# Performance work log

Hardware: AMD Instinct MI355X
Metric: run time of the kernel (lower is better)

Reference implementation:

```python
import jax, jax.numpy as jnp
import numpy as np

B, S, D_MODEL, D_K = 4, 4096, 1024, 64


def setup_inputs() -> dict:
    key = jax.random.key(0)
    kx, kq, kk, kv = jax.random.split(key, 4)
    x = jax.random.normal(kx, (B, S, D_MODEL), dtype=jnp.float32)
    # Linear(in, out) stores weight as (out, in); y = x @ W^T, no bias
    Wq = jax.random.normal(kq, (D_K, D_MODEL), dtype=jnp.float32) * (D_MODEL ** -0.5)
    Wk = jax.random.normal(kk, (D_K, D_MODEL), dtype=jnp.float32) * (D_MODEL ** -0.5)
    Wv = jax.random.normal(kv, (D_MODEL, D_MODEL), dtype=jnp.float32) * (D_MODEL ** -0.5)
    return {"x": x, "Wq": Wq, "Wk": Wk, "Wv": Wv}


def reference(x, Wq, Wk, Wv):
    # single-head scaled dot-product attention
    q = jnp.einsum('bsd,kd->bsk', x, Wq)   # [B,S,d_k]
    k = jnp.einsum('bsd,kd->bsk', x, Wk)   # [B,S,d_k]
    v = jnp.einsum('bsd,md->bsm', x, Wv)   # [B,S,d_model]
    scale = 1.0 / jnp.sqrt(jnp.asarray(q.shape[-1], q.dtype))
    scores = jnp.einsum('bqk,bsk->bqs', q, k) * scale  # [B,S,S]
    probs = jax.nn.softmax(scores, axis=-1)
    return jnp.einsum('bqs,bsm->bqm', probs, v)        # [B,S,d_model]
```

## Files before the change

kernel.cpp:

```cpp
#include <hip/hip_runtime.h>


#define DEV static __device__ __forceinline__

typedef __attribute__((ext_vector_type(8))) short bf16x8;
typedef __attribute__((ext_vector_type(4))) float f32x4;
typedef __attribute__((ext_vector_type(4))) unsigned short u16x4;
typedef __attribute__((ext_vector_type(8))) unsigned short u16x8;
typedef __attribute__((address_space(1))) void as1_void;
typedef __attribute__((address_space(3))) void as3_void;

DEV unsigned short f2bf(float f) {
  union { float f; unsigned u; } v; v.f = f;
  return (unsigned short)((v.u + 0x7FFFu + ((v.u >> 16) & 1u)) >> 16);
}

DEV unsigned pk_bf16(float a, float b) {
  union { float f; unsigned u; } va, vb;
  va.f = a; vb.f = b;
  return __builtin_amdgcn_perm(vb.u + 0x8000u, va.u + 0x8000u, 0x07060302u);
}

DEV void gload16(const void* g, void* l) {
  __builtin_amdgcn_global_load_lds((as1_void*)g, (as3_void*)l, 16, 0, 0);
}

DEV int swz(int row, int cb) { return (row << 7) + (cb ^ ((row & 7) << 4)); }

DEV void lgkm_barrier() {
  asm volatile("s_waitcnt lgkmcnt(0)" ::: "memory");
  __builtin_amdgcn_sched_barrier(0);
  __builtin_amdgcn_s_barrier();
  __builtin_amdgcn_sched_barrier(0);
}

__global__ __launch_bounds__(256) void cast_bf16_k(const float* __restrict__ in,
                                                   unsigned short* __restrict__ out,
                                                   int n8, float scale) {
  const int stride = gridDim.x * blockDim.x;
  for (int i = blockIdx.x * blockDim.x + threadIdx.x; i < n8; i += stride) {
    const float4* p = (const float4*)in + (size_t)i * 2;
    float4 a = p[0], b = p[1];
    u16x8 r;
    r[0] = f2bf(a.x * scale); r[1] = f2bf(a.y * scale);
    r[2] = f2bf(a.z * scale); r[3] = f2bf(a.w * scale);
    r[4] = f2bf(b.x * scale); r[5] = f2bf(b.y * scale);
    r[6] = f2bf(b.z * scale); r[7] = f2bf(b.w * scale);
    *(u16x8*)(out + (size_t)i * 8) = r;
  }
}

__global__ __launch_bounds__(256, 2) void gemm_qkv_k(
    const unsigned short* __restrict__ xb, const unsigned short* __restrict__ wcat,
    unsigned short* __restrict__ qk, unsigned short* __restrict__ vT) {
  __shared__ __align__(16) unsigned char smem[65536];
  unsigned char* sA = smem;
  unsigned char* sB = smem + 32768;
  const int tid = threadIdx.x;
  const int w = tid >> 6, lane = tid & 63, lo = lane & 15, hi = lane >> 4;
  const int wr = w >> 1, wc = w & 1;
  const int bn = blockIdx.x, m0 = blockIdx.y * 128, n0 = bn * 128;
  const char* aBase = (const char*)xb + (size_t)m0 * 2048;
  const char* bBase = (const char*)wcat + (size_t)n0 * 2048;

  const int soff = ((w * 4) << 10) + (lane << 4);
  f32x4 acc[4][4];
  const f32x4 z = {0.f, 0.f, 0.f, 0.f};
#pragma unroll
  for (int mi = 0; mi < 4; ++mi)
#pragma unroll
    for (int ni = 0; ni < 4; ++ni) acc[mi][ni] = z;

#pragma unroll
  for (int r2 = 0; r2 < 4; ++r2) {
    const int off = soff + (r2 << 10);
    const int row = off >> 7;
    const int cbs = (off & 127) ^ ((row & 7) << 4);
    gload16(aBase + (size_t)row * 2048 + cbs, sA + ((w * 4 + r2) << 10));
    gload16(bBase + (size_t)row * 2048 + cbs, sB + ((w * 4 + r2) << 10));
  }
  __syncthreads();

  int cur = 0;
  for (int k0 = 0; k0 < 1024; k0 += 64) {
    if (k0 + 64 < 1024) {
      const int nb = (cur ^ 1) * 16384;
#pragma unroll
      for (int r2 = 0; r2 < 4; ++r2) {
        const int off = soff + (r2 << 10);
        const int row = off >> 7;
        const int cbs = (off & 127) ^ ((row & 7) << 4);
        gload16(aBase + (size_t)row * 2048 + (k0 + 64) * 2 + cbs, sA + nb + ((w * 4 + r2) << 10));
        gload16(bBase + (size_t)row * 2048 + (k0 + 64) * 2 + cbs, sB + nb + ((w * 4 + r2) << 10));
      }
    }
    const int cb0 = cur * 16384;
#pragma unroll
    for (int kk = 0; kk < 2; ++kk) {
      const int cb = kk * 64 + hi * 16;
      bf16x8 af[4], bfv[4];
#pragma unroll
      for (int mi = 0; mi < 4; ++mi)
        af[mi] = *(const bf16x8*)(sA + cb0 + swz(wr * 64 + mi * 16 + lo, cb));
#pragma unroll
      for (int ni = 0; ni < 4; ++ni)
        bfv[ni] = *(const bf16x8*)(sB + cb0 + swz(wc * 64 + ni * 16 + lo, cb));
#pragma unroll
      for (int mi = 0; mi < 4; ++mi)
#pragma unroll
        for (int ni = 0; ni < 4; ++ni)
          acc[mi][ni] = __builtin_amdgcn_mfma_f32_16x16x32_bf16(af[mi], bfv[ni], acc[mi][ni], 0, 0, 0);
    }
    __syncthreads();
    cur ^= 1;
  }

  if (bn == 0) {
#pragma unroll
    for (int mi = 0; mi < 4; ++mi) {
      const int row = m0 + wr * 64 + mi * 16 + hi * 4;
#pragma unroll
      for (int ni = 0; ni < 4; ++ni) {
        const int col = wc * 64 + ni * 16 + lo;
#pragma unroll
        for (int r = 0; r < 4; ++r)
          qk[(size_t)(row + r) * 128 + col] = f2bf(acc[mi][ni][r]);
      }
    }
  } else {
#pragma unroll
    for (int mi = 0; mi < 4; ++mi) {
      const int grow = m0 + wr * 64 + mi * 16 + hi * 4;
      const int b = grow >> 12, s = grow & 4095;
#pragma unroll
      for (int ni = 0; ni < 4; ++ni) {
        const int vcol = (n0 - 128) + wc * 64 + ni * 16 + lo;
        u16x4 pk;
#pragma unroll
        for (int r = 0; r < 4; ++r) pk[r] = f2bf(acc[mi][ni][r]);
        *(u16x4*)(vT + (size_t)(b * 1024 + vcol) * 4096 + s) = pk;
      }
    }
  }
}

__global__ __launch_bounds__(512, 4) void pv_k(
    const unsigned short* __restrict__ qk, const unsigned short* __restrict__ vT,
    float* __restrict__ out) {
  __shared__ __align__(16) unsigned char smem[57344];
  unsigned char* sK = smem;
  unsigned char* sV = smem + 8192;
  unsigned char* sP = smem + 40960;
  const int tid = threadIdx.x;
  const int w = tid >> 6, lane = tid & 63, lo = lane & 15, hi = lane >> 4;
  const int wr = w >> 2, wc = w & 3;
  const int ck = blockIdx.x, qt = blockIdx.y, b = blockIdx.z;
  const char* qkB = (const char*)qk;
  const char* vTB = (const char*)vT;
  const size_t qrow0 = (size_t)(b * 4096 + qt * 128);
  const f32x4 z = {0.f, 0.f, 0.f, 0.f};

  const int q = w * 16 + lo;
  bf16x8 qf[2];
#pragma unroll
  for (int kk = 0; kk < 2; ++kk)
    qf[kk] = *(const bf16x8*)(qkB + (qrow0 + q) * 256 + kk * 64 + hi * 16);
  float lsum = 0.f;

  const int kc = w * 64 + lane;
  const int kRow = kc >> 3;
  const int kCbs = ((kc & 7) << 4) ^ ((kRow & 7) << 4);
  const char* kSrc = qkB + (size_t)(b * 4096 + kRow) * 256 + 128 + kCbs;

  const int g = lane & 3, dr = (lane >> 2) & 1, qq = lane >> 3;
  const int rr = (qq & 3) + ((qq >> 2) << 3) + (dr << 2);
  const int vRow0 = w * 16 + rr, vRow1 = vRow0 + 128;
  const char* vSrc0 = vTB + (size_t)(b * 1024 + ck * 256 + vRow0) * 8192 + g * 16;
  const char* vSrc1 = vTB + (size_t)(b * 1024 + ck * 256 + vRow1) * 8192 + g * 16;
  unsigned char* vDst0 = sV + vRow0 * 128;
  unsigned char* vDst1 = sV + vRow1 * 128;
  const int vX = g << 4, vR = (vRow0 & 7) << 4;

  const int qx7 = (q & 7) << 4;
  const int aP0 = (q << 7) + ((((hi >> 1) + 0) << 4) ^ qx7) + ((hi & 1) << 3);
  const int aP1 = (q << 7) + ((((hi >> 1) + 2) << 4) ^ qx7) + ((hi & 1) << 3);

  f32x4 acc[4][4];
#pragma unroll
  for (int mi = 0; mi < 4; ++mi)
#pragma unroll
    for (int ni = 0; ni < 4; ++ni) acc[mi][ni] = z;

  {
    float4 v0 = *(const float4*)(vSrc0);
    float4 v1 = *(const float4*)(vSrc1);
    if (w < 4) gload16(kSrc, sK + (w << 10));
    *(float4*)(vDst0 + (vX ^ vR)) = v0;
    *(float4*)(vDst1 + (vX ^ vR)) = v1;
  }
  __syncthreads();

  int cur = 0;
  for (int t = 0; t < 128; ++t) {
    float4 nv0, nv1;
    if (t < 127) {
      nv0 = *(const float4*)(vSrc0 + (size_t)(t + 1) * 64);
      nv1 = *(const float4*)(vSrc1 + (size_t)(t + 1) * 64);
      if (w < 4) gload16(kSrc + (size_t)(t + 1) * 8192, sK + (cur ^ 1) * 4096 + (w << 10));
    }
    f32x4 sv0 = z, sv1 = z;
#pragma unroll
    for (int kk = 0; kk < 2; ++kk) {
      bf16x8 kf0 = *(const bf16x8*)(sK + cur * 4096 + swz(lo, kk * 64 + hi * 16));
      bf16x8 kf1 = *(const bf16x8*)(sK + cur * 4096 + swz(16 + lo, kk * 64 + hi * 16));
      sv0 = __builtin_amdgcn_mfma_f32_16x16x32_bf16(kf0, qf[kk], sv0, 0, 0, 0);
      sv1 = __builtin_amdgcn_mfma_f32_16x16x32_bf16(kf1, qf[kk], sv1, 0, 0, 0);
    }
    {
      const float p0 = __builtin_amdgcn_exp2f(sv0[0]);
      const float p1 = __builtin_amdgcn_exp2f(sv0[1]);
      const float p2 = __builtin_amdgcn_exp2f(sv0[2]);
      const float p3 = __builtin_amdgcn_exp2f(sv0[3]);
      const float p4 = __builtin_amdgcn_exp2f(sv1[0]);
      const float p5 = __builtin_amdgcn_exp2f(sv1[1]);
      const float p6 = __builtin_amdgcn_exp2f(sv1[2]);
      const float p7 = __builtin_amdgcn_exp2f(sv1[3]);
      lsum += ((p0 + p1) + (p2 + p3)) + ((p4 + p5) + (p6 + p7));
      uint2 d0, d1;
      d0.x = pk_bf16(p0, p1); d0.y = pk_bf16(p2, p3);
      d1.x = pk_bf16(p4, p5); d1.y = pk_bf16(p6, p7);
      *(uint2*)(sP + aP0) = d0;
      *(uint2*)(sP + aP1) = d1;
    }
    lgkm_barrier();
    if (t < 127) {
      *(float4*)(vDst0 + ((((cur ^ 1) << 6) + vX) ^ vR)) = nv0;
      *(float4*)(vDst1 + ((((cur ^ 1) << 6) + vX) ^ vR)) = nv1;
    }
    __builtin_amdgcn_s_setprio(1);
    bf16x8 pa[4];
#pragma unroll
    for (int mi = 0; mi < 4; ++mi)
      pa[mi] = *(const bf16x8*)(sP + swz(wr * 64 + mi * 16 + lo, hi * 16));
#pragma unroll
    for (int ni = 0; ni < 4; ++ni) {
      bf16x8 vf = *(const bf16x8*)(sV + swz(wc * 64 + ni * 16 + lo, (cur << 6) + hi * 16));
#pragma unroll
      for (int mi = 0; mi < 4; ++mi)
        acc[mi][ni] = __builtin_amdgcn_mfma_f32_16x16x32_bf16(pa[mi], vf, acc[mi][ni], 0, 0, 0);
    }
    __builtin_amdgcn_s_setprio(0);
    __syncthreads();
    cur ^= 1;
  }

  lsum += __shfl_xor(lsum, 16, 64);
  lsum += __shfl_xor(lsum, 32, 64);
  float* lLds = (float*)smem;
  if (hi == 0) lLds[q] = lsum;
  __syncthreads();

#pragma unroll
  for (int mi = 0; mi < 4; ++mi)
#pragma unroll
    for (int r = 0; r < 4; ++r) {
      const int rloc = wr * 64 + mi * 16 + hi * 4 + r;
      const int grow = (int)qrow0 + rloc;
      const float linv = 1.0f / lLds[rloc];
#pragma unroll
      for (int ni = 0; ni < 4; ++ni) {
        const int col = ck * 256 + wc * 64 + ni * 16 + lo;
        out[(size_t)grow * 1024 + col] = acc[mi][ni][r] * linv;
      }
    }
}

extern "C" void kernel_launch(void* const* d_in, const int* in_sizes, int n_in,
                              void* d_out, int out_size, void* d_ws, size_t ws_size,
                              hipStream_t stream) {
  const float* x  = (const float*)d_in[0];
  const float* Wq = (const float*)d_in[1];
  const float* Wk = (const float*)d_in[2];
  const float* Wv = (const float*)d_in[3];

  char* ws = (char*)d_ws;
  unsigned short* xb    = (unsigned short*)(ws);
  unsigned short* wcat  = (unsigned short*)(ws + 33554432);
  unsigned short* qk    = (unsigned short*)(ws + 35913728);
  unsigned short* vT    = (unsigned short*)(ws + 40108032);

  const float SCALE_Q = 0.125f * 1.4426950408889634f;

  cast_bf16_k<<<2048, 256, 0, stream>>>(x, xb, 2097152, 1.0f);
  cast_bf16_k<<<32, 256, 0, stream>>>(Wq, wcat, 8192, SCALE_Q);
  cast_bf16_k<<<32, 256, 0, stream>>>(Wk, wcat + 65536, 8192, 1.0f);
  cast_bf16_k<<<512, 256, 0, stream>>>(Wv, wcat + 131072, 131072, 1.0f);

  gemm_qkv_k<<<dim3(9, 128), 256, 0, stream>>>(xb, wcat, qk, vT);
  pv_k<<<dim3(4, 32, 4), 512, 0, stream>>>(qk, vT, (float*)d_out);
}
```

Measured before the change: 253.3 us.

## Load V fragments directly into registers and remap blocks for XCD L2 locality

In the PV kernel, V tiles are no longer staged through shared memory. Each lane loads its MFMA B-operand fragments straight from global memory into double-buffered registers, which shrinks LDS from 56KB to 24KB and removes the LDS writes and reads for V. The grid is also flattened, and block indices are remapped so that blocks on the same XCD share the same (batch, column-chunk) group, meant to improve L2 reuse of K and V. The trade-off is that global loads are now less coalesced, since each lane reads 16 bytes from a different 8KB-strided row, and more registers are used.

```diff
diff --git a/kernel.cpp b/kernel.cpp
--- a/kernel.cpp
+++ b/kernel.cpp
@@ -147,14 +147,19 @@
 __global__ __launch_bounds__(512, 4) void pv_k(
     const unsigned short* __restrict__ qk, const unsigned short* __restrict__ vT,
     float* __restrict__ out) {
-  __shared__ __align__(16) unsigned char smem[57344];
+  __shared__ __align__(16) unsigned char smem[24576];
   unsigned char* sK = smem;
-  unsigned char* sV = smem + 8192;
-  unsigned char* sP = smem + 40960;
+  unsigned char* sP = smem + 8192;
   const int tid = threadIdx.x;
   const int w = tid >> 6, lane = tid & 63, lo = lane & 15, hi = lane >> 4;
   const int wr = w >> 2, wc = w & 3;
-  const int ck = blockIdx.x, qt = blockIdx.y, b = blockIdx.z;
+
+  const int flat = blockIdx.x;
+  const int xcd = flat & 7, slot = flat >> 3;
+  const int group = xcd + ((slot >> 5) << 3);
+  const int qt = slot & 31;
+  const int ck = group & 3, b = group >> 2;
+
   const char* qkB = (const char*)qk;
   const char* vTB = (const char*)vT;
   const size_t qrow0 = (size_t)(b * 4096 + qt * 128);
@@ -172,14 +177,10 @@
   const int kCbs = ((kc & 7) << 4) ^ ((kRow & 7) << 4);
   const char* kSrc = qkB + (size_t)(b * 4096 + kRow) * 256 + 128 + kCbs;
 
-  const int g = lane & 3, dr = (lane >> 2) & 1, qq = lane >> 3;
-  const int rr = (qq & 3) + ((qq >> 2) << 3) + (dr << 2);
-  const int vRow0 = w * 16 + rr, vRow1 = vRow0 + 128;
-  const char* vSrc0 = vTB + (size_t)(b * 1024 + ck * 256 + vRow0) * 8192 + g * 16;
-  const char* vSrc1 = vTB + (size_t)(b * 1024 + ck * 256 + vRow1) * 8192 + g * 16;
-  unsigned char* vDst0 = sV + vRow0 * 128;
-  unsigned char* vDst1 = sV + vRow1 * 128;
-  const int vX = g << 4, vR = (vRow0 & 7) << 4;
+  const char* vBase[4];
+#pragma unroll
+  for (int ni = 0; ni < 4; ++ni)
+    vBase[ni] = vTB + (size_t)(b * 1024 + ck * 256 + wc * 64 + ni * 16 + lo) * 8192 + hi * 16;
 
   const int qx7 = (q & 7) << 4;
   const int aP0 = (q << 7) + ((((hi >> 1) + 0) << 4) ^ qx7) + ((hi & 1) << 3);
@@ -191,68 +192,66 @@
 #pragma unroll
     for (int ni = 0; ni < 4; ++ni) acc[mi][ni] = z;
 
-  {
-    float4 v0 = *(const float4*)(vSrc0);
-    float4 v1 = *(const float4*)(vSrc1);
-    if (w < 4) gload16(kSrc, sK + (w << 10));
-    *(float4*)(vDst0 + (vX ^ vR)) = v0;
-    *(float4*)(vDst1 + (vX ^ vR)) = v1;
-  }
+  bf16x8 vA[4], vB[4];
+#pragma unroll
+  for (int ni = 0; ni < 4; ++ni) vA[ni] = *(const bf16x8*)(vBase[ni]);
+  if (w < 4) gload16(kSrc, sK + (w << 10));
   __syncthreads();
 
-  int cur = 0;
-  for (int t = 0; t < 128; ++t) {
-    float4 nv0, nv1;
-    if (t < 127) {
-      nv0 = *(const float4*)(vSrc0 + (size_t)(t + 1) * 64);
-      nv1 = *(const float4*)(vSrc1 + (size_t)(t + 1) * 64);
-      if (w < 4) gload16(kSrc + (size_t)(t + 1) * 8192, sK + (cur ^ 1) * 4096 + (w << 10));
-    }
-    f32x4 sv0 = z, sv1 = z;
-#pragma unroll
-    for (int kk = 0; kk < 2; ++kk) {
-      bf16x8 kf0 = *(const bf16x8*)(sK + cur * 4096 + swz(lo, kk * 64 + hi * 16));
-      bf16x8 kf1 = *(const bf16x8*)(sK + cur * 4096 + swz(16 + lo, kk * 64 + hi * 16));
-      sv0 = __builtin_amdgcn_mfma_f32_16x16x32_bf16(kf0, qf[kk], sv0, 0, 0, 0);
-      sv1 = __builtin_amdgcn_mfma_f32_16x16x32_bf16(kf1, qf[kk], sv1, 0, 0, 0);
-    }
-    {
-      const float p0 = __builtin_amdgcn_exp2f(sv0[0]);
-      const float p1 = __builtin_amdgcn_exp2f(sv0[1]);
-      const float p2 = __builtin_amdgcn_exp2f(sv0[2]);
-      const float p3 = __builtin_amdgcn_exp2f(sv0[3]);
-      const float p4 = __builtin_amdgcn_exp2f(sv1[0]);
-      const float p5 = __builtin_amdgcn_exp2f(sv1[1]);
-      const float p6 = __builtin_amdgcn_exp2f(sv1[2]);
-      const float p7 = __builtin_amdgcn_exp2f(sv1[3]);
-      lsum += ((p0 + p1) + (p2 + p3)) + ((p4 + p5) + (p6 + p7));
-      uint2 d0, d1;
-      d0.x = pk_bf16(p0, p1); d0.y = pk_bf16(p2, p3);
-      d1.x = pk_bf16(p4, p5); d1.y = pk_bf16(p6, p7);
-      *(uint2*)(sP + aP0) = d0;
-      *(uint2*)(sP + aP1) = d1;
-    }
-    lgkm_barrier();
-    if (t < 127) {
-      *(float4*)(vDst0 + ((((cur ^ 1) << 6) + vX) ^ vR)) = nv0;
-      *(float4*)(vDst1 + ((((cur ^ 1) << 6) + vX) ^ vR)) = nv1;
-    }
-    __builtin_amdgcn_s_setprio(1);
-    bf16x8 pa[4];
-#pragma unroll
-    for (int mi = 0; mi < 4; ++mi)
-      pa[mi] = *(const bf16x8*)(sP + swz(wr * 64 + mi * 16 + lo, hi * 16));
-#pragma unroll
-    for (int ni = 0; ni < 4; ++ni) {
-      bf16x8 vf = *(const bf16x8*)(sV + swz(wc * 64 + ni * 16 + lo, (cur << 6) + hi * 16));
-#pragma unroll
-      for (int mi = 0; mi < 4; ++mi)
-        acc[mi][ni] = __builtin_amdgcn_mfma_f32_16x16x32_bf16(pa[mi], vf, acc[mi][ni], 0, 0, 0);
-    }
-    __builtin_amdgcn_s_setprio(0);
-    __syncthreads();
-    cur ^= 1;
-  }
+#define PV_TILE(T, CURB, VU, VL)                                                      \
+  {                                                                                   \
+    if ((T) + 1 < 128) {                                                              \
+      const size_t toff = (size_t)((T) + 1) * 64;                                     \
+      _Pragma("unroll")                                                               \
+      for (int ni = 0; ni < 4; ++ni) VL[ni] = *(const bf16x8*)(vBase[ni] + toff);     \
+      if (w < 4)                                                                      \
+        gload16(kSrc + (size_t)((T) + 1) * 8192, sK + ((CURB) ^ 1) * 4096 + (w << 10)); \
+    }                                                                                 \
+    f32x4 sv0 = z, sv1 = z;                                                           \
+    _Pragma("unroll")                                                                 \
+    for (int kk = 0; kk < 2; ++kk) {                                                  \
+      bf16x8 kf0 = *(const bf16x8*)(sK + (CURB) * 4096 + swz(lo, kk * 64 + hi * 16)); \
+      bf16x8 kf1 = *(const bf16x8*)(sK + (CURB) * 4096 + swz(16 + lo, kk * 64 + hi * 16)); \
+      sv0 = __builtin_amdgcn_mfma_f32_16x16x32_bf16(kf0, qf[kk], sv0, 0, 0, 0);       \
+      sv1 = __builtin_amdgcn_mfma_f32_16x16x32_bf16(kf1, qf[kk], sv1, 0, 0, 0);       \
+    }                                                                                 \
+    {                                                                                 \
+      const float p0 = __builtin_amdgcn_exp2f(sv0[0]);                                \
+      const float p1 = __builtin_amdgcn_exp2f(sv0[1]);                                \
+      const float p2 = __builtin_amdgcn_exp2f(sv0[2]);                                \
+      const float p3 = __builtin_amdgcn_exp2f(sv0[3]);                                \
+      const float p4 = __builtin_amdgcn_exp2f(sv1[0]);                                \
+      const float p5 = __builtin_amdgcn_exp2f(sv1[1]);                                \
+      const float p6 = __builtin_amdgcn_exp2f(sv1[2]);                                \
+      const float p7 = __builtin_amdgcn_exp2f(sv1[3]);                                \
+      lsum += ((p0 + p1) + (p2 + p3)) + ((p4 + p5) + (p6 + p7));                      \
+      uint2 d0, d1;                                                                   \
+      d0.x = pk_bf16(p0, p1); d0.y = pk_bf16(p2, p3);                                 \
+      d1.x = pk_bf16(p4, p5); d1.y = pk_bf16(p6, p7);                                 \
+      *(uint2*)(sP + aP0) = d0;                                                       \
+      *(uint2*)(sP + aP1) = d1;                                                       \
+    }                                                                                 \
+    lgkm_barrier();                                                                   \
+    __builtin_amdgcn_s_setprio(1);                                                    \
+    bf16x8 pa[4];                                                                     \
+    _Pragma("unroll")                                                                 \
+    for (int mi = 0; mi < 4; ++mi)                                                    \
+      pa[mi] = *(const bf16x8*)(sP + swz(wr * 64 + mi * 16 + lo, hi * 16));           \
+    _Pragma("unroll")                                                                 \
+    for (int ni = 0; ni < 4; ++ni) {                                                  \
+      _Pragma("unroll")                                                               \
+      for (int mi = 0; mi < 4; ++mi)                                                  \
+        acc[mi][ni] = __builtin_amdgcn_mfma_f32_16x16x32_bf16(pa[mi], VU[ni], acc[mi][ni], 0, 0, 0); \
+    }                                                                                 \
+    __builtin_amdgcn_s_setprio(0);                                                    \
+    __syncthreads();                                                                  \
+  }
+
+  for (int t2 = 0; t2 < 128; t2 += 2) {
+    PV_TILE(t2,     0, vA, vB);
+    PV_TILE(t2 + 1, 1, vB, vA);
+  }
+#undef PV_TILE
 
   lsum += __shfl_xor(lsum, 16, 64);
   lsum += __shfl_xor(lsum, 32, 64);
@@ -297,5 +296,5 @@
   cast_bf16_k<<<512, 256, 0, stream>>>(Wv, wcat + 131072, 131072, 1.0f);
 
   gemm_qkv_k<<<dim3(9, 128), 256, 0, stream>>>(xb, wcat, qk, vT);
-  pv_k<<<dim3(4, 32, 4), 512, 0, stream>>>(qk, vT, (float*)d_out);
-}
+  pv_k<<<512, 512, 0, stream>>>(qk, vT, (float*)d_out);
+}
```

Measured after the change: 887.3 us. +250.3%, slower.
